# Performance work log

Hardware: AMD Instinct MI355X
Metric: run time of the kernel (lower is better)

Reference implementation:

```python
import jax, jax.numpy as jnp
import numpy as np

IMG = 48
N = IMG * IMG          # 2304 oscillators
B = 4
STEPS = 4              # cfg['kuramoto_steps']
K_COUP = 1.0           # cfg['coupling_K']
DT = 0.1               # cfg['dt']
ALPHA_SCALE = 1.0      # cfg['lag_scale']
BN_EPS = 1e-5


def _conv2d(x, w, b, pad):
    # x: [B,C,H,W], w: [O,I,kh,kw]
    y = jax.lax.conv_general_dilated(
        x, w, window_strides=(1, 1), padding=[(pad, pad), (pad, pad)],
        dimension_numbers=('NCHW', 'OIHW', 'NCHW'))
    return y + b[None, :, None, None]


def setup_inputs() -> dict:
    key = jax.random.key(0)
    ks = jax.random.split(key, 12)
    inp = {
        'x': jax.random.normal(ks[0], (B, 1, IMG, IMG), jnp.float32),
        'conv1_w': jax.random.normal(ks[1], (16, 1, 3, 3), jnp.float32) * 0.2,
        'conv1_b': jax.random.normal(ks[2], (16,), jnp.float32) * 0.05,
        'bn_gamma': jnp.ones((16,), jnp.float32),
        'bn_beta': jnp.zeros((16,), jnp.float32),
        'conv2_w': jax.random.normal(ks[3], (16, 16, 3, 3), jnp.float32) * 0.1,
        'conv2_b': jax.random.normal(ks[4], (16,), jnp.float32) * 0.05,
        'feat_w': jax.random.normal(ks[5], (8, 16, 1, 1), jnp.float32) * 0.2,
        'feat_b': jax.random.normal(ks[6], (8,), jnp.float32) * 0.05,
        'drive_w': jax.random.normal(ks[7], (1, 16, 1, 1), jnp.float32) * 0.2,
        'drive_b': jax.random.normal(ks[8], (1,), jnp.float32) * 0.05,
        'omega': jax.random.normal(ks[9], (N, 1), jnp.float32) * 0.1,
        'kappa': jnp.ones((N, 1), jnp.float32),
        'direction_learner': jax.random.normal(ks[10], (N, N), jnp.float32) * 0.01,
        'theta0': jax.random.uniform(ks[11], (B, N, 1), jnp.float32) * (2.0 * np.pi),
    }
    return inp


def reference(x, conv1_w, conv1_b, bn_gamma, bn_beta, conv2_w, conv2_b,
              feat_w, feat_b, drive_w, drive_b, omega, kappa,
              direction_learner, theta0):
    # ---- backbone: conv -> BN (batch stats, train mode) -> tanh -> conv -> tanh
    h = _conv2d(x, conv1_w, conv1_b, pad=1)
    mu = jnp.mean(h, axis=(0, 2, 3), keepdims=True)
    var = jnp.mean((h - mu) ** 2, axis=(0, 2, 3), keepdims=True)  # biased var, torch BN
    h = bn_gamma[None, :, None, None] * (h - mu) / jnp.sqrt(var + BN_EPS) \
        + bn_beta[None, :, None, None]
    h = jnp.tanh(h)
    h = jnp.tanh(_conv2d(h, conv2_w, conv2_b, pad=1))

    # ---- heads
    gamma = _conv2d(h, drive_w, drive_b, pad=0).reshape(B, N)          # [B,N]
    feat = _conv2d(h, feat_w, feat_b, pad=0).reshape(B, 8, N)
    feat = jnp.transpose(feat, (0, 2, 1))                              # [B,N,8]
    fnorm = feat / jnp.maximum(
        jnp.sqrt(jnp.sum(feat * feat, axis=2, keepdims=True)), 1e-12)

    # ---- cosine-similarity connectivity, zero diagonal
    A = jnp.einsum('bnd,bmd->bnm', fnorm, fnorm)                       # [B,N,N]
    A = A * (1.0 - jnp.eye(N, dtype=A.dtype))

    # ---- OT-derived phase lag (constant across steps, so hoisted)
    A_lat = jax.nn.relu(0.5 * (A + jnp.transpose(A, (0, 2, 1)))) + 1e-6
    cost = 1.0 / A_lat
    c_min = jnp.min(cost, axis=(1, 2), keepdims=True)
    c_max = jnp.max(cost, axis=(1, 2), keepdims=True)
    norm_cost = (cost - c_min) / (c_max - c_min + 1e-6)
    direction = jnp.tanh(direction_learner - direction_learner.T)      # antisym -> tanh
    alpha = ALPHA_SCALE * direction[None, :, :] * norm_cost            # [B,N,N]

    # ---- Kuramoto integration (D=1, work in [B,N])
    theta = theta0[..., 0]
    om = omega[:, 0][None, :]
    kp = kappa[:, 0][None, :]
    for _ in range(STEPS):
        # phase_diff[b,i,j] = theta_j - theta_i - alpha_ij
        pd = theta[:, None, :] - theta[:, :, None] - alpha             # [B,N,N]
        interaction = jnp.sum(A_lat * jnp.sin(pd), axis=2)             # [B,N]
        coupling = (K_COUP / float(N)) * interaction
        drive_term = kp * jnp.sin(gamma - theta)
        theta = theta + DT * (om + coupling + drive_term)
    return theta  # [B,N]
```

## Files before the change

kernel.cpp:

```cpp
#include <hip/hip_runtime.h>
#include <hip/hip_fp16.h>

#define IMG 48
#define NPIX 2304
#define NB 4
#define NCH 16
#define DT 0.1f
#define BN_EPS 1e-5f
#define TPB 576
#define GRID_BLKS 256

typedef _Float16 h2v __attribute__((ext_vector_type(2)));
typedef unsigned long long u64;

#if defined(__has_builtin)
#if __has_builtin(__builtin_amdgcn_fdot2)
#define HAVE_FDOT2 1
#endif
#endif

__device__ __forceinline__ void ast32(unsigned* p, unsigned v) {
    __hip_atomic_store(p, v, __ATOMIC_RELAXED, __HIP_MEMORY_SCOPE_AGENT);
}
__device__ __forceinline__ unsigned ald32(const unsigned* p) {
    return __hip_atomic_load(p, __ATOMIC_RELAXED, __HIP_MEMORY_SCOPE_AGENT);
}
__device__ __forceinline__ void ast_u64(void* p, u64 v) {
    __hip_atomic_store((u64*)p, v, __ATOMIC_RELAXED, __HIP_MEMORY_SCOPE_AGENT);
}
__device__ __forceinline__ u64 ald_u64(const void* p) {
    return __hip_atomic_load((const u64*)p, __ATOMIC_RELAXED, __HIP_MEMORY_SCOPE_AGENT);
}
__device__ __forceinline__ u64 pack2f(float a, float b) {
    return (u64)__float_as_uint(a) | ((u64)__float_as_uint(b) << 32);
}

__shared__ __align__(16) char smem[58368];

__device__ __forceinline__ void fbar_all(unsigned* flags, unsigned* gen, unsigned ph) {
    __syncthreads();
    if (threadIdx.x == 0) ast32(&flags[blockIdx.x], ph);
    if (blockIdx.x == 0) {
        if (threadIdx.x < 64) {
            for (;;) {
                int ok = 1;
                #pragma unroll
                for (int k = 0; k < 4; ++k)
                    ok &= (ald32(&flags[threadIdx.x + 64 * k]) >= ph) ? 1 : 0;
                if (__all(ok)) break;
                __builtin_amdgcn_s_sleep(1);
            }
            if (threadIdx.x == 0) ast32(&gen[4 * 16], ph);
        }
    } else if (threadIdx.x == 0) {
        while (ald32(&gen[4 * 16]) < ph) __builtin_amdgcn_s_sleep(2);
    }
    __syncthreads();
}
__device__ __forceinline__ void fbar_batch(unsigned* flags, unsigned* gen,
                                           unsigned ph, int sb) {
    __syncthreads();
    if (threadIdx.x == 0) ast32(&flags[blockIdx.x], ph);
    if (blockIdx.x == (sb << 6)) {
        if (threadIdx.x < 64) {
            const unsigned* f = flags + (sb << 6);
            for (;;) {
                int ok = (ald32(&f[threadIdx.x]) >= ph) ? 1 : 0;
                if (__all(ok)) break;
                __builtin_amdgcn_s_sleep(1);
            }
            if (threadIdx.x == 0) ast32(&gen[sb * 16], ph);
        }
    } else if (threadIdx.x == 0) {
        while (ald32(&gen[sb * 16]) < ph) __builtin_amdgcn_s_sleep(2);
    }
    __syncthreads();
}

__device__ __forceinline__ float dot8(const h2v fi[4], uint4 w) {
#ifdef HAVE_FDOT2
    float d = __builtin_amdgcn_fdot2(fi[0], __builtin_bit_cast(h2v, w.x), 0.0f, false);
    d = __builtin_amdgcn_fdot2(fi[1], __builtin_bit_cast(h2v, w.y), d, false);
    d = __builtin_amdgcn_fdot2(fi[2], __builtin_bit_cast(h2v, w.z), d, false);
    d = __builtin_amdgcn_fdot2(fi[3], __builtin_bit_cast(h2v, w.w), d, false);
    return d;
#else
    float d = 0.f;
    unsigned ws[4] = {w.x, w.y, w.z, w.w};
    #pragma unroll
    for (int k = 0; k < 4; ++k) {
        h2v a = fi[k], b = __builtin_bit_cast(h2v, ws[k]);
        d += (float)a.x * (float)b.x + (float)a.y * (float)b.y;
    }
    return d;
#endif
}

__global__ __launch_bounds__(TPB, 2) void k_all(
    const float* __restrict__ x,  const float* __restrict__ w1, const float* __restrict__ b1,
    const float* __restrict__ bng, const float* __restrict__ bnb,
    const float* __restrict__ w2, const float* __restrict__ b2,
    const float* __restrict__ fw, const float* __restrict__ fbv,
    const float* __restrict__ dw, const float* __restrict__ dbv,
    const float* __restrict__ om, const float* __restrict__ kp,
    const float* __restrict__ th0, float* __restrict__ out,
    unsigned* __restrict__ flags, unsigned* __restrict__ gen,
    u64* __restrict__ partials, u64* __restrict__ fnorm_h, float2* __restrict__ gam2,
    u64* __restrict__ uv0, u64* __restrict__ uv1)
{
    const int tid  = threadIdx.x;
    const int blk  = blockIdx.x;
    const int wave = tid >> 6, lane = tid & 63;
    const int sb   = blk >> 6;
    const int base = (blk & 63) * 36;
    const int trow0 = base / IMG - 1;

    float*  sw2p = (float*)smem;
    float*  ht   = (float*)(smem + 9280);
    float*  h2s  = (float*)(smem + 22144);
    float*  p0red= (float*)(smem + 24448);
    float*  redc = (float*)(smem + 25600);
    float2* bnred= (float2*)(smem + 25728);

    {
        const float* xb = x + sb * NPIX;
        if (tid < 128) {
            int ch = tid >> 3, r4 = (tid >> 1) & 3, side = tid & 1;
            ht[ch * 201 + r4 * 50 + side * 49] = 0.f;
        }
        #pragma unroll
        for (int k = 0; k < 6; ++k) {
            int idx = tid + k * TPB;
            if (idx < 3072) {
                int ch = idx / 192, rc = idx % 192;
                int tr = rc / 48, col = rc % 48;
                int y = trow0 + tr;
                float s = 0.f;
                if (y >= 0 && y < IMG) {
                    s = b1[ch];
                    #pragma unroll
                    for (int ky = 0; ky < 3; ++ky) {
                        int yy = y + ky - 1;
                        if (yy < 0 || yy >= IMG) continue;
                        #pragma unroll
                        for (int kx = 0; kx < 3; ++kx) {
                            int x2 = col + kx - 1;
                            if (x2 < 0 || x2 >= IMG) continue;
                            s += xb[yy * IMG + x2] * w1[ch * 9 + ky * 3 + kx];
                        }
                    }
                }
                ht[ch * 201 + tr * 50 + col + 1] = s;
            }
        }
        __syncthreads();
        int lpx = tid >> 4, oc = tid & 15;
        int p = base + lpx;
        int tr = p / IMG - trow0, col = p % IMG;
        float v = ht[oc * 201 + tr * 50 + col + 1];
        float S = v, Q = v * v;
        S += __shfl_down(S, 32, 64); Q += __shfl_down(Q, 32, 64);
        S += __shfl_down(S, 16, 64); Q += __shfl_down(Q, 16, 64);
        if (lane < 16) { p0red[wave * 32 + lane * 2] = S; p0red[wave * 32 + lane * 2 + 1] = Q; }
        __syncthreads();
        if (tid < 16) {
            float Ss = 0.f, Qs = 0.f;
            #pragma unroll
            for (int w8 = 0; w8 < 9; ++w8) {
                Ss += p0red[w8 * 32 + tid * 2];
                Qs += p0red[w8 * 32 + tid * 2 + 1];
            }
            ast_u64(&partials[blk * 16 + tid], pack2f(Ss, Qs));
        }
    }
    fbar_all(flags, gen, 1);

    {
        if (tid < 512) {
            int c = tid >> 5, g = tid & 31;
            u64 vv[8];
            #pragma unroll
            for (int k = 0; k < 8; ++k) vv[k] = ald_u64(&partials[(g * 8 + k) * 16 + c]);
            float S = 0.f, Q = 0.f;
            #pragma unroll
            for (int k = 0; k < 8; ++k) {
                S += __uint_as_float((unsigned)vv[k]);
                Q += __uint_as_float((unsigned)(vv[k] >> 32));
            }
            bnred[c * 32 + g] = make_float2(S, Q);
        }
        for (int k = tid; k < NCH * NCH * 9; k += TPB) {
            int o = k / 144, r = k - o * 144;
            sw2p[o * 145 + r] = w2[k];
        }
        __syncthreads();
        if (tid < 16) {
            float S = 0.f, Q = 0.f;
            #pragma unroll
            for (int g = 0; g < 32; ++g) { S += bnred[tid * 32 + g].x; Q += bnred[tid * 32 + g].y; }
            const float inv_n = 1.0f / (float)(NB * NPIX);
            float mu = S * inv_n, var = Q * inv_n - mu * mu;
            float sc = bng[tid] * rsqrtf(var + BN_EPS);
            redc[tid * 2] = sc; redc[tid * 2 + 1] = bnb[tid] - mu * sc;
        }
        __syncthreads();
        #pragma unroll
        for (int k = 0; k < 6; ++k) {
            int idx = tid + k * TPB;
            if (idx < 3072) {
                int ch = idx / 192, rc = idx % 192;
                int tr = rc / 48, col = rc % 48;
                int y = trow0 + tr;
                if (y >= 0 && y < IMG) {
                    int a = ch * 201 + tr * 50 + col + 1;
                    ht[a] = tanhf(fmaf(ht[a], redc[ch * 2], redc[ch * 2 + 1]));
                }
            }
        }
        __syncthreads();

        int lpx = tid >> 4, oc = tid & 15;
        int p = base + lpx;
        int y = p / IMG, cx = p % IMG;
        int tr1 = y - trow0;
        float acc = b2[oc];
        const float* wrow = &sw2p[oc * 145];
        #pragma unroll 4
        for (int ic = 0; ic < 16; ++ic) {
            const float* hrow = &ht[ic * 201];
            #pragma unroll
            for (int ky = 0; ky < 3; ++ky) {
                int rr = (tr1 + ky - 1) * 50 + cx;
                #pragma unroll
                for (int kx = 0; kx < 3; ++kx)
                    acc += hrow[rr + kx] * wrow[ic * 9 + ky * 3 + kx];
            }
        }
        float h2val = tanhf(acc);
        h2s[tid] = h2val;
        __syncthreads();
        int bgrp = tid & ~15;
        int px = blk * 36 + lpx;
        if (oc < 8) {
            float f = fbv[oc];
            #pragma unroll
            for (int o2 = 0; o2 < 16; ++o2) f += fw[oc * 16 + o2] * h2s[bgrp + o2];
            float ssq = f * f;
            ssq += __shfl_xor(ssq, 1, 16);
            ssq += __shfl_xor(ssq, 2, 16);
            ssq += __shfl_xor(ssq, 4, 16);
            unsigned hb = (unsigned)__half_as_ushort(
                __float2half(f * (1.0f / fmaxf(sqrtf(ssq), 1e-12f))));
            unsigned g0 = __shfl(hb, (lane & ~3) | 0, 64);
            unsigned g1 = __shfl(hb, (lane & ~3) | 1, 64);
            unsigned g2 = __shfl(hb, (lane & ~3) | 2, 64);
            unsigned g3 = __shfl(hb, (lane & ~3) | 3, 64);
            if ((oc & 3) == 0) {
                u64 pk = (u64)g0 | ((u64)g1 << 16) | ((u64)g2 << 32) | ((u64)g3 << 48);
                ast_u64(&fnorm_h[px * 2 + (oc >> 2)], pk);
            }
        } else if (oc == 15) {
            float g = dbv[0];
            #pragma unroll
            for (int o2 = 0; o2 < 16; ++o2) g += dw[o2] * h2s[bgrp + o2];
            float k_ = kp[p];
            float sg, cg; __sincosf(g, &sg, &cg);
            gam2[px] = make_float2(k_ * sg, k_ * cg);
        }
    }

    {
        uint4*  sfn4 = (uint4*)smem;
        float2* suv  = (float2*)(smem + 38912);
        const int li0 = (blk & 63) * 36 + wave * 4;

        fbar_batch(flags, gen, 2, sb);

        const u64* fng = fnorm_h + (size_t)sb * NPIX * 2;
        const float* th0b = th0 + sb * NPIX;
        u64 ra[4], rb[4]; float tv[4];
        #pragma unroll
        for (int k = 0; k < 4; ++k) {
            int e = tid + k * TPB;
            ra[k] = ald_u64(&fng[e * 2]);
            rb[k] = ald_u64(&fng[e * 2 + 1]);
            tv[k] = th0b[e];
        }
        #pragma unroll
        for (int k = 0; k < 4; ++k) {
            int e = tid + k * TPB;
            sfn4[e] = make_uint4((unsigned)ra[k], (unsigned)(ra[k] >> 32),
                                 (unsigned)rb[k], (unsigned)(rb[k] >> 32));
            float sn, cn; __sincosf(tv[k], &sn, &cn);
            suv[e] = make_float2(sn, cn);
        }
        __syncthreads();

        h2v fi[4][4]; float thi[4];
        #pragma unroll
        for (int r = 0; r < 4; ++r) {
            uint4 w = sfn4[li0 + r];
            fi[r][0] = __builtin_bit_cast(h2v, w.x);
            fi[r][1] = __builtin_bit_cast(h2v, w.y);
            fi[r][2] = __builtin_bit_cast(h2v, w.z);
            fi[r][3] = __builtin_bit_cast(h2v, w.w);
            thi[r] = th0b[li0 + r];
        }

        for (int s = 0; s < 4; ++s) {
            if (s > 0) {
                const u64* uvg = ((s & 1) ? uv1 : uv0) + sb * NPIX;
                u64 ru[4];
                #pragma unroll
                for (int k = 0; k < 4; ++k) ru[k] = ald_u64(&uvg[tid + k * TPB]);
                #pragma unroll
                for (int k = 0; k < 4; ++k)
                    suv[tid + k * TPB] = make_float2(
                        __uint_as_float((unsigned)ru[k]),
                        __uint_as_float((unsigned)(ru[k] >> 32)));
                __syncthreads();
            }

            float a1[4] = {0.f,0.f,0.f,0.f}, a2[4] = {0.f,0.f,0.f,0.f};
            uint4  w0 = sfn4[lane],      wA = sfn4[64 + lane];
            float2 U0 = suv[lane],       UA = suv[64 + lane];
            #pragma unroll 4
            for (int tt = 0; tt < NPIX / 64; ++tt) {
                uint4  wn = sfn4[(tt + 2) * 64 + lane];
                float2 Un = suv[(tt + 2) * 64 + lane];
                #pragma unroll
                for (int r = 0; r < 4; ++r) {
                    float al = fmaxf(dot8(fi[r], w0), 0.f);
                    a1[r] = fmaf(al, U0.x, a1[r]);
                    a2[r] = fmaf(al, U0.y, a2[r]);
                }
                w0 = wA; U0 = UA; wA = wn; UA = Un;
            }
            #pragma unroll
            for (int o = 32; o; o >>= 1) {
                #pragma unroll
                for (int r = 0; r < 4; ++r) {
                    a1[r] += __shfl_down(a1[r], o, 64);
                    a2[r] += __shfl_down(a2[r], o, 64);
                }
            }
            if (lane == 0) {
                #pragma unroll
                for (int r = 0; r < 4; ++r) {
                    int i = li0 + r, row = sb * NPIX + i;
                    float2 uvi = suv[i];
                    float inter = uvi.y * a1[r] - uvi.x * a2[r];
                    float2 g2 = gam2[row];
                    float drv = g2.x * uvi.y - g2.y * uvi.x;
                    float tn = thi[r] + DT * (om[i] + inter * (1.0f / (float)NPIX) + drv);
                    thi[r] = tn;
                    if (s == 3) {
                        out[row] = tn;
                    } else {
                        float sn, cn; __sincosf(tn, &sn, &cn);
                        ast_u64(&(((s & 1) ? uv0 : uv1)[row]), pack2f(sn, cn));
                    }
                }
            }
            if (s < 3) fbar_batch(flags, gen, 3 + s, sb);
        }
    }
}

extern "C" void kernel_launch(void* const* d_in, const int* in_sizes, int n_in,
                              void* d_out, int out_size, void* d_ws, size_t ws_size,
                              hipStream_t stream) {
    const float* x   = (const float*)d_in[0];
    const float* w1  = (const float*)d_in[1];
    const float* b1  = (const float*)d_in[2];
    const float* bng = (const float*)d_in[3];
    const float* bnb = (const float*)d_in[4];
    const float* w2  = (const float*)d_in[5];
    const float* b2  = (const float*)d_in[6];
    const float* fw  = (const float*)d_in[7];
    const float* fb  = (const float*)d_in[8];
    const float* dw  = (const float*)d_in[9];
    const float* db  = (const float*)d_in[10];
    const float* om  = (const float*)d_in[11];
    const float* kp  = (const float*)d_in[12];
    const float* th0 = (const float*)d_in[14];
    float* out = (float*)d_out;

    char* wsb = (char*)d_ws;
    unsigned* flags   = (unsigned*)wsb;
    unsigned* gen     = (unsigned*)(wsb + 1024);
    u64*      partials= (u64*)(wsb + 1536);
    u64*      fnorm_h = (u64*)(wsb + 34304);
    float2*   gam2    = (float2*)(wsb + 181760);
    u64*      uv0     = (u64*)(wsb + 255488);
    u64*      uv1     = (u64*)(wsb + 329216);

    hipMemsetAsync(wsb, 0, 1536, stream);

    k_all<<<dim3(GRID_BLKS), dim3(TPB), 0, stream>>>(
        x, w1, b1, bng, bnb, w2, b2, fw, fb, dw, db, om, kp, th0, out,
        flags, gen, partials, fnorm_h, gam2, uv0, uv1);
}
```

Baseline: 65.09 us.

## Replace per-batch grid barriers with chunked flag waits overlapping compute

Removes the centralized per-batch barrier (master block polls, then broadcasts a generation word). Each block now waits directly on the flags of the 16 producer blocks that own each quarter of the oscillators, then stages and consumes that quarter right away. Arrival of later chunks can therefore overlap work on earlier ones. Shared memory use drops because phases are staged per chunk and the per-row sin/cos, omega and drive values are kept in registers. The cost is more flag polling by every block and more __syncthreads per step.

```diff
diff --git a/kernel.cpp b/kernel.cpp
--- a/kernel.cpp
+++ b/kernel.cpp
@@ -35,7 +35,7 @@
     return (u64)__float_as_uint(a) | ((u64)__float_as_uint(b) << 32);
 }
 
-__shared__ __align__(16) char smem[58368];
+__shared__ __align__(16) char smem[41472];
 
 __device__ __forceinline__ void fbar_all(unsigned* flags, unsigned* gen, unsigned ph) {
     __syncthreads();
@@ -50,29 +50,10 @@
                 if (__all(ok)) break;
                 __builtin_amdgcn_s_sleep(1);
             }
-            if (threadIdx.x == 0) ast32(&gen[4 * 16], ph);
+            if (threadIdx.x == 0) ast32(&gen[64], ph);
         }
     } else if (threadIdx.x == 0) {
-        while (ald32(&gen[4 * 16]) < ph) __builtin_amdgcn_s_sleep(2);
-    }
-    __syncthreads();
-}
-__device__ __forceinline__ void fbar_batch(unsigned* flags, unsigned* gen,
-                                           unsigned ph, int sb) {
-    __syncthreads();
-    if (threadIdx.x == 0) ast32(&flags[blockIdx.x], ph);
-    if (blockIdx.x == (sb << 6)) {
-        if (threadIdx.x < 64) {
-            const unsigned* f = flags + (sb << 6);
-            for (;;) {
-                int ok = (ald32(&f[threadIdx.x]) >= ph) ? 1 : 0;
-                if (__all(ok)) break;
-                __builtin_amdgcn_s_sleep(1);
-            }
-            if (threadIdx.x == 0) ast32(&gen[sb * 16], ph);
-        }
-    } else if (threadIdx.x == 0) {
-        while (ald32(&gen[sb * 16]) < ph) __builtin_amdgcn_s_sleep(2);
+        while (ald32(&gen[64]) < ph) __builtin_amdgcn_s_sleep(2);
     }
     __syncthreads();
 }
@@ -268,73 +249,72 @@
             gam2[px] = make_float2(k_ * sg, k_ * cg);
         }
     }
+    __syncthreads();
+    if (tid == 0) ast32(&flags[blk], 2);
 
     {
-        uint4*  sfn4 = (uint4*)smem;
-        float2* suv  = (float2*)(smem + 38912);
+        uint4*  sfn4  = (uint4*)smem;
+        float2* svbuf = (float2*)(smem + 36864);
         const int li0 = (blk & 63) * 36 + wave * 4;
-
-        fbar_batch(flags, gen, 2, sb);
-
         const u64* fng = fnorm_h + (size_t)sb * NPIX * 2;
         const float* th0b = th0 + sb * NPIX;
-        u64 ra[4], rb[4]; float tv[4];
-        #pragma unroll
-        for (int k = 0; k < 4; ++k) {
-            int e = tid + k * TPB;
-            ra[k] = ald_u64(&fng[e * 2]);
-            rb[k] = ald_u64(&fng[e * 2 + 1]);
-            tv[k] = th0b[e];
-        }
-        #pragma unroll
-        for (int k = 0; k < 4; ++k) {
-            int e = tid + k * TPB;
-            sfn4[e] = make_uint4((unsigned)ra[k], (unsigned)(ra[k] >> 32),
-                                 (unsigned)rb[k], (unsigned)(rb[k] >> 32));
-            float sn, cn; __sincosf(tv[k], &sn, &cn);
-            suv[e] = make_float2(sn, cn);
-        }
-        __syncthreads();
-
-        h2v fi[4][4]; float thi[4];
+
+        h2v fi[4][4]; float thi[4], omr[4], us[4], uc[4]; float2 g2r[4];
         #pragma unroll
         for (int r = 0; r < 4; ++r) {
-            uint4 w = sfn4[li0 + r];
-            fi[r][0] = __builtin_bit_cast(h2v, w.x);
-            fi[r][1] = __builtin_bit_cast(h2v, w.y);
-            fi[r][2] = __builtin_bit_cast(h2v, w.z);
-            fi[r][3] = __builtin_bit_cast(h2v, w.w);
-            thi[r] = th0b[li0 + r];
+            int i = li0 + r;
+            u64 a = ald_u64(&fng[i * 2]), b = ald_u64(&fng[i * 2 + 1]);
+            fi[r][0] = __builtin_bit_cast(h2v, (unsigned)a);
+            fi[r][1] = __builtin_bit_cast(h2v, (unsigned)(a >> 32));
+            fi[r][2] = __builtin_bit_cast(h2v, (unsigned)b);
+            fi[r][3] = __builtin_bit_cast(h2v, (unsigned)(b >> 32));
+            thi[r] = th0b[i];
+            omr[r] = om[i];
+            g2r[r] = gam2[sb * NPIX + i];
+            __sincosf(thi[r], &us[r], &uc[r]);
         }
 
         for (int s = 0; s < 4; ++s) {
-            if (s > 0) {
-                const u64* uvg = ((s & 1) ? uv1 : uv0) + sb * NPIX;
-                u64 ru[4];
-                #pragma unroll
-                for (int k = 0; k < 4; ++k) ru[k] = ald_u64(&uvg[tid + k * TPB]);
-                #pragma unroll
-                for (int k = 0; k < 4; ++k)
-                    suv[tid + k * TPB] = make_float2(
-                        __uint_as_float((unsigned)ru[k]),
-                        __uint_as_float((unsigned)(ru[k] >> 32)));
+            const unsigned need = (s == 0) ? 2u : (unsigned)(2 + s);
+            const u64* uvsrc = (((s - 1) & 1) ? uv1 : uv0) + sb * NPIX;
+            float a1[4] = {0.f,0.f,0.f,0.f}, a2[4] = {0.f,0.f,0.f,0.f};
+
+            for (int g = 0; g < 4; ++g) {
+                if (tid < 64) {
+                    const unsigned* f = flags + (sb << 6) + (g << 4);
+                    for (;;) {
+                        int ok = (tid < 16) ? (ald32(&f[tid]) >= need) : 1;
+                        if (__all(ok)) break;
+                        __builtin_amdgcn_s_sleep(1);
+                    }
+                }
                 __syncthreads();
-            }
-
-            float a1[4] = {0.f,0.f,0.f,0.f}, a2[4] = {0.f,0.f,0.f,0.f};
-            uint4  w0 = sfn4[lane],      wA = sfn4[64 + lane];
-            float2 U0 = suv[lane],       UA = suv[64 + lane];
-            #pragma unroll 4
-            for (int tt = 0; tt < NPIX / 64; ++tt) {
-                uint4  wn = sfn4[(tt + 2) * 64 + lane];
-                float2 Un = suv[(tt + 2) * 64 + lane];
-                #pragma unroll
-                for (int r = 0; r < 4; ++r) {
-                    float al = fmaxf(dot8(fi[r], w0), 0.f);
-                    a1[r] = fmaf(al, U0.x, a1[r]);
-                    a2[r] = fmaf(al, U0.y, a2[r]);
-                }
-                w0 = wA; U0 = UA; wA = wn; UA = Un;
+                int e = g * 576 + tid;
+                if (s == 0) {
+                    u64 a = ald_u64(&fng[e * 2]);
+                    u64 b = ald_u64(&fng[e * 2 + 1]);
+                    sfn4[e] = make_uint4((unsigned)a, (unsigned)(a >> 32),
+                                         (unsigned)b, (unsigned)(b >> 32));
+                    float sn, cn; __sincosf(th0b[e], &sn, &cn);
+                    svbuf[tid] = make_float2(sn, cn);
+                } else {
+                    u64 u = ald_u64(&uvsrc[e]);
+                    svbuf[tid] = make_float2(__uint_as_float((unsigned)u),
+                                             __uint_as_float((unsigned)(u >> 32)));
+                }
+                __syncthreads();
+                #pragma unroll 3
+                for (int t2 = 0; t2 < 9; ++t2) {
+                    int jl = t2 * 64 + lane;
+                    uint4 w = sfn4[g * 576 + jl];
+                    float2 U = svbuf[jl];
+                    #pragma unroll
+                    for (int r = 0; r < 4; ++r) {
+                        float al = fmaxf(dot8(fi[r], w), 0.f);
+                        a1[r] = fmaf(al, U.x, a1[r]);
+                        a2[r] = fmaf(al, U.y, a2[r]);
+                    }
+                }
             }
             #pragma unroll
             for (int o = 32; o; o >>= 1) {
@@ -347,22 +327,24 @@
             if (lane == 0) {
                 #pragma unroll
                 for (int r = 0; r < 4; ++r) {
-                    int i = li0 + r, row = sb * NPIX + i;
-                    float2 uvi = suv[i];
-                    float inter = uvi.y * a1[r] - uvi.x * a2[r];
-                    float2 g2 = gam2[row];
-                    float drv = g2.x * uvi.y - g2.y * uvi.x;
-                    float tn = thi[r] + DT * (om[i] + inter * (1.0f / (float)NPIX) + drv);
+                    int row = sb * NPIX + li0 + r;
+                    float inter = uc[r] * a1[r] - us[r] * a2[r];
+                    float drv = g2r[r].x * uc[r] - g2r[r].y * us[r];
+                    float tn = thi[r] + DT * (omr[r] + inter * (1.0f / (float)NPIX) + drv);
                     thi[r] = tn;
                     if (s == 3) {
                         out[row] = tn;
                     } else {
                         float sn, cn; __sincosf(tn, &sn, &cn);
-                        ast_u64(&(((s & 1) ? uv0 : uv1)[row]), pack2f(sn, cn));
+                        us[r] = sn; uc[r] = cn;
+                        ast_u64(&(((s & 1) ? uv1 : uv0)[row]), pack2f(sn, cn));
                     }
                 }
             }
-            if (s < 3) fbar_batch(flags, gen, 3 + s, sb);
+            if (s < 3) {
+                __syncthreads();
+                if (tid == 0) ast32(&flags[blk], 3 + s);
+            }
         }
     }
 }
```

Result: slower. 66.98 us (+2.9%).
